# Kernel optimization log

Hardware: AMD Instinct MI355X
Metric: run time of the kernel (lower is better)

Reference implementation:

```python
import jax, jax.numpy as jnp
import numpy as np

B, S, D, H = 2, 2048, 1024, 16
DK = D // H
NEG = -1.0e9


def setup_inputs() -> dict:
    key = jax.random.key(0)
    ks = jax.random.split(key, 11)
    inp = {
        "q": jax.random.normal(ks[0], (B, S, D), jnp.float32),
        "k": jax.random.normal(ks[1], (B, S, D), jnp.float32),
        "v": jax.random.normal(ks[2], (B, S, D), jnp.float32),
        "mask": jnp.tril(jnp.ones((S, S), jnp.int32))[None, None],  # causal [1,1,S,S]
    }
    scale = 0.02
    inp["w_q"] = jax.random.normal(ks[3], (D, D), jnp.float32) * scale
    inp["b_q"] = jnp.zeros((D,), jnp.float32)
    inp["w_k"] = jax.random.normal(ks[4], (D, D), jnp.float32) * scale
    inp["b_k"] = jnp.zeros((D,), jnp.float32)
    inp["w_v"] = jax.random.normal(ks[5], (D, D), jnp.float32) * scale
    inp["b_v"] = jnp.zeros((D,), jnp.float32)
    inp["w_o"] = jax.random.normal(ks[6], (D, D), jnp.float32) * scale
    inp["b_o"] = jnp.zeros((D,), jnp.float32)
    return inp


def reference(q, k, v, mask, w_q, b_q, w_k, b_k, w_v, b_v, w_o, b_o):
    # projections: [B,S,D] -> [B,H,S,DK]
    def proj(x, w, b):
        y = jnp.einsum("bsd,de->bse", x, w) + b
        return y.reshape(B, S, H, DK).transpose(0, 2, 1, 3)

    Q = proj(q, w_q, b_q)
    K = proj(k, w_k, b_k)
    V = proj(v, w_v, b_v)
    # explicit scores matrix, faithful to the original naive attention
    scores = jnp.einsum("bhsd,bhtd->bhst", Q, K) / jnp.sqrt(jnp.float32(DK))
    scores = jnp.where(mask == 0, NEG, scores)
    attn = jax.nn.softmax(scores, axis=-1)  # dropout p=0.0 -> identity
    x = jnp.einsum("bhst,bhtd->bhsd", attn, V)
    x = x.transpose(0, 2, 1, 3).reshape(B, S, D)
    return jnp.einsum("bsd,de->bse", x, w_o) + b_o
```

## Files before the change

### kernel.cpp

```cpp
#include <hip/hip_runtime.h>
#include <hip/hip_bf16.h>

typedef __bf16 bf16;
typedef __bf16 bf16x2 __attribute__((ext_vector_type(2)));
typedef __bf16 bf16x8 __attribute__((ext_vector_type(8)));
typedef float f32x4 __attribute__((ext_vector_type(4)));
typedef float f32x16 __attribute__((ext_vector_type(16)));

#define MFMA16(a, b, c) __builtin_amdgcn_mfma_f32_16x16x32_bf16(a, b, c, 0, 0, 0)
#define MFMA32(a, b, c) __builtin_amdgcn_mfma_f32_32x32x16_bf16(a, b, c, 0, 0, 0)

#define QSCALE 0.18033688f

__global__ __launch_bounds__(256) void convert_k(const float* __restrict__ q,
                                                 const float* __restrict__ k,
                                                 const float* __restrict__ v,
                                                 bf16* __restrict__ qb,
                                                 bf16* __restrict__ kb,
                                                 bf16* __restrict__ vb) {
  const float* src = blockIdx.y == 0 ? q : blockIdx.y == 1 ? k : v;
  bf16* dst = blockIdx.y == 0 ? qb : blockIdx.y == 1 ? kb : vb;
  const size_t i = ((size_t)blockIdx.x * 256 + threadIdx.x) * 8;
  float4 a = *(const float4*)(src + i);
  float4 b = *(const float4*)(src + i + 4);
  bf16x8 o;
  o[0] = (bf16)a.x; o[1] = (bf16)a.y; o[2] = (bf16)a.z; o[3] = (bf16)a.w;
  o[4] = (bf16)b.x; o[5] = (bf16)b.y; o[6] = (bf16)b.z; o[7] = (bf16)b.w;
  *(bf16x8*)(dst + i) = o;
}

__global__ __launch_bounds__(256) void transpose_w(const float* __restrict__ w0,
                                                   const float* __restrict__ w1,
                                                   const float* __restrict__ w2,
                                                   const float* __restrict__ w3,
                                                   bf16* __restrict__ dst) {
  __shared__ bf16 T[64][68];
  const float* W = blockIdx.z == 0 ? w0 : blockIdx.z == 1 ? w1
                   : blockIdx.z == 2 ? w2 : w3;
  bf16* Y = dst + (size_t)blockIdx.z * 1024 * 1024;
  const int t = threadIdx.x, r = t >> 2, c4 = t & 3;
  const int k0 = blockIdx.y * 64, n0 = blockIdx.x * 64;

  const float4* src = (const float4*)(W + (size_t)(k0 + r) * 1024 + n0 + c4 * 16);
  float4 f0 = src[0], f1 = src[1], f2 = src[2], f3 = src[3];
  bf16* row = &T[r][c4 * 16];
  row[0] = (bf16)f0.x; row[1] = (bf16)f0.y; row[2] = (bf16)f0.z; row[3] = (bf16)f0.w;
  row[4] = (bf16)f1.x; row[5] = (bf16)f1.y; row[6] = (bf16)f1.z; row[7] = (bf16)f1.w;
  row[8] = (bf16)f2.x; row[9] = (bf16)f2.y; row[10] = (bf16)f2.z; row[11] = (bf16)f2.w;
  row[12] = (bf16)f3.x; row[13] = (bf16)f3.y; row[14] = (bf16)f3.z; row[15] = (bf16)f3.w;
  __syncthreads();

  bf16x8 o0, o1;
#pragma unroll
  for (int j = 0; j < 8; ++j) o0[j] = T[c4 * 16 + j][r];
#pragma unroll
  for (int j = 0; j < 8; ++j) o1[j] = T[c4 * 16 + 8 + j][r];
  bf16* d = Y + (size_t)(n0 + r) * 1024 + k0 + c4 * 16;
  *(bf16x8*)d = o0;
  *(bf16x8*)(d + 8) = o1;
}

template <int QKV, int MT>
__global__ __launch_bounds__(256, 3) void gemm_p(
    const bf16* __restrict__ xq, const bf16* __restrict__ xk,
    const bf16* __restrict__ xv, const bf16* __restrict__ Wt,
    const float* __restrict__ bq, const float* __restrict__ bk,
    const float* __restrict__ bv, bf16* __restrict__ Qp,
    bf16* __restrict__ Kp, bf16* __restrict__ Vtp, float* __restrict__ Yf) {
  constexpr int AROWS = MT * 32;
  __shared__ bf16 Al[AROWS * 72];
  __shared__ bf16 Bl[128 * 72];

  const int z = QKV ? blockIdx.z : 0;
  const bf16* X = QKV ? (z == 0 ? xq : z == 1 ? xk : xv) : xq;
  const bf16* Bt = Wt + (size_t)z * 1048576;
  const float* bias = QKV ? (z == 0 ? bq : z == 1 ? bk : bv) : bq;
  const float escale = (QKV && z == 0) ? QSCALE : 1.0f;

  const int t = threadIdx.x;
  const int wave = t >> 6, lane = t & 63, quad = lane >> 4, l16 = lane & 15;
  const int wm = (wave >> 1) * (MT * 16), wn = (wave & 1) * 64;
  const int bm = blockIdx.y * AROWS, bn = blockIdx.x * 128;

  constexpr int NA = (MT == 4) ? 4 : 2;
  const int arow = (MT == 4) ? (t >> 1) : (t >> 2);
  const int acol = (MT == 4) ? ((t & 1) * 32) : ((t & 3) * 16);
  const int brow = t >> 1, bcol = (t & 1) * 32;
  const bf16* gA = X + (size_t)(bm + arow) * 1024 + acol;
  const bf16* gB = Bt + (size_t)(bn + brow) * 1024 + bcol;

  bf16x8 ra[NA], rb[4];
#pragma unroll
  for (int j = 0; j < NA; ++j) ra[j] = *(const bf16x8*)(gA + j * 8);
#pragma unroll
  for (int j = 0; j < 4; ++j) rb[j] = *(const bf16x8*)(gB + j * 8);

  f32x4 acc[MT][4] = {};

  for (int kb = 0; kb < 1024; kb += 64) {
    __syncthreads();
#pragma unroll
    for (int j = 0; j < NA; ++j)
      *(bf16x8*)(Al + arow * 72 + acol + j * 8) = ra[j];
#pragma unroll
    for (int j = 0; j < 4; ++j)
      *(bf16x8*)(Bl + brow * 72 + bcol + j * 8) = rb[j];
    __syncthreads();

    if (kb + 64 < 1024) {
#pragma unroll
      for (int j = 0; j < NA; ++j)
        ra[j] = *(const bf16x8*)(gA + kb + 64 + j * 8);
#pragma unroll
      for (int j = 0; j < 4; ++j)
        rb[j] = *(const bf16x8*)(gB + kb + 64 + j * 8);
    }

#pragma unroll
    for (int kk = 0; kk < 2; ++kk) {
      bf16x8 af[MT], bfr[4];
#pragma unroll
      for (int mt = 0; mt < MT; ++mt)
        af[mt] =
            *(const bf16x8*)(Al + (wm + mt * 16 + l16) * 72 + kk * 32 + quad * 8);
#pragma unroll
      for (int nt = 0; nt < 4; ++nt)
        bfr[nt] =
            *(const bf16x8*)(Bl + (wn + nt * 16 + l16) * 72 + kk * 32 + quad * 8);
#pragma unroll
      for (int mt = 0; mt < MT; ++mt)
#pragma unroll
        for (int nt = 0; nt < 4; ++nt)
          acc[mt][nt] = MFMA16(af[mt], bfr[nt], acc[mt][nt]);
    }
  }

  if (QKV && z == 2) {
    bf16* Tt = Al;
    const int b = bm >> 11;
    __syncthreads();
#pragma unroll
    for (int half = 0; half < 2; ++half) {
      if ((wave & 1) == half) {
#pragma unroll
        for (int nt = 0; nt < 4; ++nt) {
          const int ln = nt * 16 + l16;
          const float bia = bias[bn + half * 64 + ln];
#pragma unroll
          for (int mt = 0; mt < 4; ++mt)
#pragma unroll
            for (int r = 0; r < 4; ++r) {
              const int m = wm + mt * 16 + quad * 4 + r;
              Tt[ln * 136 + m] = (bf16)(acc[mt][nt][r] + bia);
            }
        }
      }
      __syncthreads();
      {
        const int ln = t >> 2, seg = (t & 3) * 32;
        const int gn = bn + half * 64 + ln;
        const int h = gn >> 6, dk = gn & 63;
        const int s0 = (bm & 2047) + seg;
        bf16* dstp = Vtp + ((size_t)(b * 16 + h) * 64 + dk) * 2048 + s0;
        const bf16* srcp = Tt + ln * 136 + seg;
#pragma unroll
        for (int j = 0; j < 4; ++j)
          *(bf16x8*)(dstp + j * 8) = *(const bf16x8*)(srcp + j * 8);
      }
      __syncthreads();
    }
  } else {
#pragma unroll
    for (int mt = 0; mt < MT; ++mt)
#pragma unroll
      for (int nt = 0; nt < 4; ++nt) {
        const int gn = bn + wn + nt * 16 + l16;
        const float bia = bias[gn];
#pragma unroll
        for (int r = 0; r < 4; ++r) {
          const int gm = bm + wm + mt * 16 + quad * 4 + r;
          const float val = (acc[mt][nt][r] + bia) * escale;
          if (!QKV) {
            Yf[(size_t)gm * 1024 + gn] = val;
          } else {
            const int b = gm >> 11, s = gm & 2047;
            const int h = gn >> 6, dk = gn & 63;
            bf16* Y = (z == 0) ? Qp : Kp;
            Y[((size_t)(b * 16 + h) * 2048 + s) * 64 + dk] = (bf16)val;
          }
        }
      }
  }
}

__global__ __launch_bounds__(256, 2) void attn_k(const bf16* __restrict__ Q,
                                                 const bf16* __restrict__ K,
                                                 const bf16* __restrict__ Vt,
                                                 bf16* __restrict__ X) {
  __shared__ __align__(16) bf16 Kl[2][64 * 64];
  __shared__ __align__(16) bf16 Vl[2][64 * 64];
  __shared__ float rsL[4][32];

  const int t = threadIdx.x;
  const int wave = t >> 6, lane = t & 63;
  const int cl = lane & 31, h = lane >> 5;

  const int n = blockIdx.x;
  const int xcd = n & 7, mm = n >> 3;
  const int bh = xcd + 8 * (mm & 3);
  const int ii = mm >> 2;
  const int qt = (ii < 8) ? ii : 23 - ii;
  const int ntiles = 2 * qt + 2;
  const int q0 = qt * 128 + wave * 32;
  const int b = bh >> 4, hh = bh & 15;

  const bf16* Qb = Q + (size_t)bh * 2048 * 64;
  const bf16* Kb = K + (size_t)bh * 2048 * 64;
  const bf16* Vb = Vt + (size_t)bh * 64 * 2048;

  bf16x8 qf[4];
#pragma unroll
  for (int ks = 0; ks < 4; ++ks)
    qf[ks] = *(const bf16x8*)(Qb + (size_t)(q0 + cl) * 64 + ks * 16 + h * 8);

  const int sr = t >> 2, sc4 = t & 3;
  const int swz = (sr & 7) << 4;
  const int d0 = sr * 128 + ((sc4 * 32) ^ swz);
  const int d1 = sr * 128 + ((sc4 * 32 + 16) ^ swz);
  const bf16* gK = Kb + sr * 64 + sc4 * 16;
  const bf16* gV = Vb + (size_t)sr * 2048 + sc4 * 16;

  const int fswz = (cl & 7) << 4;

  f32x16 o0 = {}, o1 = {};
  float rs = 0.f;

  {
    bf16x8 ka = *(const bf16x8*)gK;
    bf16x8 kb2 = *(const bf16x8*)(gK + 8);
    bf16x8 va = *(const bf16x8*)gV;
    bf16x8 vb2 = *(const bf16x8*)(gV + 8);
    *(bf16x8*)((char*)Kl[0] + d0) = ka;
    *(bf16x8*)((char*)Kl[0] + d1) = kb2;
    *(bf16x8*)((char*)Vl[0] + d0) = va;
    *(bf16x8*)((char*)Vl[0] + d1) = vb2;
  }
  __syncthreads();

  for (int kt = 0; kt < ntiles; ++kt) {
    const int cur = kt & 1;
    const int k0 = kt * 64;
    const bool more = kt + 1 < ntiles;
    bf16x8 ka, kb2, va, vb2;
    if (more) {
      const bf16* nK = gK + (size_t)(kt + 1) * 4096;
      const bf16* nV = gV + (kt + 1) * 64;
      ka = *(const bf16x8*)nK;
      kb2 = *(const bf16x8*)(nK + 8);
      va = *(const bf16x8*)nV;
      vb2 = *(const bf16x8*)(nV + 8);
    }

    f32x16 s0 = {}, s1 = {};
    const char* Kc = (const char*)Kl[cur];
    __builtin_amdgcn_s_setprio(1);
#pragma unroll
    for (int ks = 0; ks < 4; ++ks) {
      const int cb = ks * 32 + h * 16;
      bf16x8 f0 = *(const bf16x8*)(Kc + cl * 128 + (cb ^ fswz));
      bf16x8 f1 = *(const bf16x8*)(Kc + (cl + 32) * 128 + (cb ^ fswz));
      s0 = MFMA32(f0, qf[ks], s0);
      s1 = MFMA32(f1, qf[ks], s1);
    }
    __builtin_amdgcn_s_setprio(0);

    const bool interior = (k0 + 63) <= q0;
    unsigned pk[8][2];
    float ts = 0.f;
    auto smax = [&](const f32x16& s, int mk) {
#pragma unroll
      for (int sl = 0; sl < 4; ++sl)
#pragma unroll
        for (int p = 0; p < 2; ++p) {
          float e0 = exp2f(s[sl * 4 + 2 * p]);
          float e1 = exp2f(s[sl * 4 + 2 * p + 1]);
          if (!interior) {
            const int ky = k0 + mk * 32 + 8 * sl + 4 * h + 2 * p;
            const int qg = q0 + cl;
            if (ky > qg) e0 = 0.f;
            if (ky + 1 > qg) e1 = 0.f;
          }
          ts += e0 + e1;
          union { bf16x2 v; unsigned u; } cv;
          cv.v[0] = (bf16)e0;
          cv.v[1] = (bf16)e1;
          pk[mk * 4 + sl][p] = cv.u;
        }
    };
    smax(s0, 0);
    smax(s1, 1);
    rs += ts;

    bf16x8 pf[4];
#pragma unroll
    for (int ks = 0; ks < 4; ++ks) {
      const unsigned oe0 = pk[2 * ks][0], oe1 = pk[2 * ks][1];
      const unsigned oo0 = pk[2 * ks + 1][0], oo1 = pk[2 * ks + 1][1];
      const unsigned pe0 = (unsigned)__shfl_xor((int)oe0, 32, 64);
      const unsigned pe1 = (unsigned)__shfl_xor((int)oe1, 32, 64);
      const unsigned po0 = (unsigned)__shfl_xor((int)oo0, 32, 64);
      const unsigned po1 = (unsigned)__shfl_xor((int)oo1, 32, 64);
      union { unsigned u[4]; bf16x8 v; } fu;
      fu.u[0] = h ? po0 : oe0;
      fu.u[1] = h ? po1 : oe1;
      fu.u[2] = h ? oo0 : pe0;
      fu.u[3] = h ? oo1 : pe1;
      pf[ks] = fu.v;
    }

    const char* Vc = (const char*)Vl[cur];
    __builtin_amdgcn_s_setprio(1);
#pragma unroll
    for (int ks = 0; ks < 4; ++ks) {
      const int cb = ks * 32 + h * 16;
      bf16x8 v0f = *(const bf16x8*)(Vc + cl * 128 + (cb ^ fswz));
      bf16x8 v1f = *(const bf16x8*)(Vc + (cl + 32) * 128 + (cb ^ fswz));
      o0 = MFMA32(pf[ks], v0f, o0);
      o1 = MFMA32(pf[ks], v1f, o1);
    }
    __builtin_amdgcn_s_setprio(0);

    if (more) {
      char* Kd = (char*)Kl[cur ^ 1];
      char* Vd = (char*)Vl[cur ^ 1];
      *(bf16x8*)(Kd + d0) = ka;
      *(bf16x8*)(Kd + d1) = kb2;
      *(bf16x8*)(Vd + d0) = va;
      *(bf16x8*)(Vd + d1) = vb2;
    }
    __syncthreads();
  }

  const float rtot = rs + __shfl_xor(rs, 32, 64);
  rsL[wave][cl] = 1.0f / rtot;
  __builtin_amdgcn_s_waitcnt(0xC07F);
  bf16* Xb = X + (size_t)b * 2048 * 1024 + hh * 64;
#pragma unroll
  for (int g = 0; g < 16; ++g) {
    const int qr = (g & 3) + 8 * (g >> 2) + 4 * h;
    const float ri = rsL[wave][qr];
    const int qg = q0 + qr;
    Xb[(size_t)qg * 1024 + cl] = (bf16)(o0[g] * ri);
    Xb[(size_t)qg * 1024 + 32 + cl] = (bf16)(o1[g] * ri);
  }
}

extern "C" void kernel_launch(void* const* d_in, const int* in_sizes, int n_in,
                              void* d_out, int out_size, void* d_ws,
                              size_t ws_size, hipStream_t stream) {
  const float* q = (const float*)d_in[0];
  const float* k = (const float*)d_in[1];
  const float* v = (const float*)d_in[2];
  const float* w_q = (const float*)d_in[4];
  const float* b_q = (const float*)d_in[5];
  const float* w_k = (const float*)d_in[6];
  const float* b_k = (const float*)d_in[7];
  const float* w_v = (const float*)d_in[8];
  const float* b_v = (const float*)d_in[9];
  const float* w_o = (const float*)d_in[10];
  const float* b_o = (const float*)d_in[11];

  bf16* ws = (bf16*)d_ws;
  const size_t NELEM = (size_t)4096 * 1024;
  bf16* Qp = ws;
  bf16* Kp = ws + NELEM;
  bf16* Vtp = ws + 2 * NELEM;
  bf16* Xp = ws + 3 * NELEM;
  bf16* Wt = ws + 4 * NELEM;
  bf16* Wto = Wt + 3145728;
  bf16* qb = Xp;
  bf16* kb = (bf16*)d_out;
  bf16* vb = kb + NELEM;

  convert_k<<<dim3(2048, 3), 256, 0, stream>>>(q, k, v, qb, kb, vb);
  transpose_w<<<dim3(16, 16, 4), 256, 0, stream>>>(w_q, w_k, w_v, w_o, Wt);

  gemm_p<1, 4><<<dim3(8, 32, 3), 256, 0, stream>>>(
      qb, kb, vb, Wt, b_q, b_k, b_v, Qp, Kp, Vtp, nullptr);
  attn_k<<<dim3(512), 256, 0, stream>>>(Qp, Kp, Vtp, Xp);
  gemm_p<0, 2><<<dim3(8, 64), 256, 0, stream>>>(
      Xp, nullptr, nullptr, Wto, b_o, nullptr, nullptr, nullptr, nullptr,
      nullptr, (float*)d_out);
}
```

Baseline: 248.7 us.

## Split attention KV range across wave pairs with paired causal query tiles

Restructures the attention kernel so each block handles 64-row query tiles in two phases, pairing tile i with tile 31-i to balance causal work. Waves are split into two query sub-tiles times two KV halves: each wave pair processes alternating KV tiles, and partial outputs and row sums are merged through shared memory. The aim is more parallelism per query row and better load balance. The cost is extra LDS use (about 72KB), extra barriers and reduction traffic, and the removal of the setprio hints.

```diff
diff --git a/kernel.cpp b/kernel.cpp
--- a/kernel.cpp
+++ b/kernel.cpp
@@ -197,161 +197,202 @@
                                                  const bf16* __restrict__ K,
                                                  const bf16* __restrict__ Vt,
                                                  bf16* __restrict__ X) {
-  __shared__ __align__(16) bf16 Kl[2][64 * 64];
-  __shared__ __align__(16) bf16 Vl[2][64 * 64];
+  __shared__ __align__(16) char LB[65536];
+  __shared__ float Ex[2048];
+  __shared__ float ExR[128];
   __shared__ float rsL[4][32];
+
+  bf16* KB = (bf16*)LB;
+  bf16* VB = (bf16*)(LB + 32768);
 
   const int t = threadIdx.x;
   const int wave = t >> 6, lane = t & 63;
   const int cl = lane & 31, h = lane >> 5;
+  const int qsub = wave & 1, kpart = wave >> 1;
 
   const int n = blockIdx.x;
   const int xcd = n & 7, mm = n >> 3;
   const int bh = xcd + 8 * (mm & 3);
-  const int ii = mm >> 2;
-  const int qt = (ii < 8) ? ii : 23 - ii;
-  const int ntiles = 2 * qt + 2;
-  const int q0 = qt * 128 + wave * 32;
+  const int pairx = mm >> 2;
   const int b = bh >> 4, hh = bh & 15;
 
   const bf16* Qb = Q + (size_t)bh * 2048 * 64;
   const bf16* Kb = K + (size_t)bh * 2048 * 64;
   const bf16* Vb = Vt + (size_t)bh * 64 * 2048;
-
-  bf16x8 qf[4];
-#pragma unroll
-  for (int ks = 0; ks < 4; ++ks)
-    qf[ks] = *(const bf16x8*)(Qb + (size_t)(q0 + cl) * 64 + ks * 16 + h * 8);
 
   const int sr = t >> 2, sc4 = t & 3;
   const int swz = (sr & 7) << 4;
   const int d0 = sr * 128 + ((sc4 * 32) ^ swz);
   const int d1 = sr * 128 + ((sc4 * 32 + 16) ^ swz);
-  const bf16* gK = Kb + sr * 64 + sc4 * 16;
-  const bf16* gV = Vb + (size_t)sr * 2048 + sc4 * 16;
-
   const int fswz = (cl & 7) << 4;
 
-  f32x16 o0 = {}, o1 = {};
-  float rs = 0.f;
-
-  {
-    bf16x8 ka = *(const bf16x8*)gK;
-    bf16x8 kb2 = *(const bf16x8*)(gK + 8);
-    bf16x8 va = *(const bf16x8*)gV;
-    bf16x8 vb2 = *(const bf16x8*)(gV + 8);
-    *(bf16x8*)((char*)Kl[0] + d0) = ka;
-    *(bf16x8*)((char*)Kl[0] + d1) = kb2;
-    *(bf16x8*)((char*)Vl[0] + d0) = va;
-    *(bf16x8*)((char*)Vl[0] + d1) = vb2;
-  }
-  __syncthreads();
-
-  for (int kt = 0; kt < ntiles; ++kt) {
-    const int cur = kt & 1;
-    const int k0 = kt * 64;
-    const bool more = kt + 1 < ntiles;
-    bf16x8 ka, kb2, va, vb2;
-    if (more) {
-      const bf16* nK = gK + (size_t)(kt + 1) * 4096;
-      const bf16* nV = gV + (kt + 1) * 64;
-      ka = *(const bf16x8*)nK;
-      kb2 = *(const bf16x8*)(nK + 8);
-      va = *(const bf16x8*)nV;
-      vb2 = *(const bf16x8*)(nV + 8);
-    }
-
-    f32x16 s0 = {}, s1 = {};
-    const char* Kc = (const char*)Kl[cur];
-    __builtin_amdgcn_s_setprio(1);
-#pragma unroll
-    for (int ks = 0; ks < 4; ++ks) {
-      const int cb = ks * 32 + h * 16;
-      bf16x8 f0 = *(const bf16x8*)(Kc + cl * 128 + (cb ^ fswz));
-      bf16x8 f1 = *(const bf16x8*)(Kc + (cl + 32) * 128 + (cb ^ fswz));
-      s0 = MFMA32(f0, qf[ks], s0);
-      s1 = MFMA32(f1, qf[ks], s1);
-    }
-    __builtin_amdgcn_s_setprio(0);
-
-    const bool interior = (k0 + 63) <= q0;
-    unsigned pk[8][2];
-    float ts = 0.f;
-    auto smax = [&](const f32x16& s, int mk) {
-#pragma unroll
-      for (int sl = 0; sl < 4; ++sl)
+  for (int ph = 0; ph < 2; ++ph) {
+    const int qt = ph ? 31 - pairx : pairx;
+    const int ntiles = qt + 1;
+    const int S = (ntiles + 1) >> 1;
+    const int q0 = qt * 64 + qsub * 32;
+
+    bf16x8 qf[4];
+#pragma unroll
+    for (int ks = 0; ks < 4; ++ks)
+      qf[ks] = *(const bf16x8*)(Qb + (size_t)(q0 + cl) * 64 + ks * 16 + h * 8);
+
+    f32x16 o0 = {}, o1 = {};
+    float rs = 0.f;
+
+#pragma unroll
+    for (int p = 0; p < 2; ++p) {
+      const bf16* gk = Kb + (size_t)(p * 64 + sr) * 64 + sc4 * 16;
+      const bf16* gv = Vb + (size_t)sr * 2048 + p * 64 + sc4 * 16;
+      bf16x8 ka = *(const bf16x8*)gk, kb2 = *(const bf16x8*)(gk + 8);
+      bf16x8 va = *(const bf16x8*)gv, vb2 = *(const bf16x8*)(gv + 8);
+      char* Kd = (char*)(KB + p * 4096);
+      char* Vd = (char*)(VB + p * 4096);
+      *(bf16x8*)(Kd + d0) = ka;  *(bf16x8*)(Kd + d1) = kb2;
+      *(bf16x8*)(Vd + d0) = va;  *(bf16x8*)(Vd + d1) = vb2;
+    }
+    __syncthreads();
+
+    for (int ss = 0; ss < S; ++ss) {
+      const int par = ss & 1;
+      const bool more = (ss + 1) < S;
+      bf16x8 rk[2][2], rv[2][2];
+      if (more) {
 #pragma unroll
         for (int p = 0; p < 2; ++p) {
-          float e0 = exp2f(s[sl * 4 + 2 * p]);
-          float e1 = exp2f(s[sl * 4 + 2 * p + 1]);
-          if (!interior) {
-            const int ky = k0 + mk * 32 + 8 * sl + 4 * h + 2 * p;
-            const int qg = q0 + cl;
-            if (ky > qg) e0 = 0.f;
-            if (ky + 1 > qg) e1 = 0.f;
-          }
-          ts += e0 + e1;
-          union { bf16x2 v; unsigned u; } cv;
-          cv.v[0] = (bf16)e0;
-          cv.v[1] = (bf16)e1;
-          pk[mk * 4 + sl][p] = cv.u;
-        }
-    };
-    smax(s0, 0);
-    smax(s1, 1);
-    rs += ts;
-
-    bf16x8 pf[4];
-#pragma unroll
-    for (int ks = 0; ks < 4; ++ks) {
-      const unsigned oe0 = pk[2 * ks][0], oe1 = pk[2 * ks][1];
-      const unsigned oo0 = pk[2 * ks + 1][0], oo1 = pk[2 * ks + 1][1];
-      const unsigned pe0 = (unsigned)__shfl_xor((int)oe0, 32, 64);
-      const unsigned pe1 = (unsigned)__shfl_xor((int)oe1, 32, 64);
-      const unsigned po0 = (unsigned)__shfl_xor((int)oo0, 32, 64);
-      const unsigned po1 = (unsigned)__shfl_xor((int)oo1, 32, 64);
-      union { unsigned u[4]; bf16x8 v; } fu;
-      fu.u[0] = h ? po0 : oe0;
-      fu.u[1] = h ? po1 : oe1;
-      fu.u[2] = h ? oo0 : pe0;
-      fu.u[3] = h ? oo1 : pe1;
-      pf[ks] = fu.v;
-    }
-
-    const char* Vc = (const char*)Vl[cur];
-    __builtin_amdgcn_s_setprio(1);
-#pragma unroll
-    for (int ks = 0; ks < 4; ++ks) {
-      const int cb = ks * 32 + h * 16;
-      bf16x8 v0f = *(const bf16x8*)(Vc + cl * 128 + (cb ^ fswz));
-      bf16x8 v1f = *(const bf16x8*)(Vc + (cl + 32) * 128 + (cb ^ fswz));
-      o0 = MFMA32(pf[ks], v0f, o0);
-      o1 = MFMA32(pf[ks], v1f, o1);
-    }
-    __builtin_amdgcn_s_setprio(0);
-
-    if (more) {
-      char* Kd = (char*)Kl[cur ^ 1];
-      char* Vd = (char*)Vl[cur ^ 1];
-      *(bf16x8*)(Kd + d0) = ka;
-      *(bf16x8*)(Kd + d1) = kb2;
-      *(bf16x8*)(Vd + d0) = va;
-      *(bf16x8*)(Vd + d1) = vb2;
-    }
-    __syncthreads();
-  }
-
-  const float rtot = rs + __shfl_xor(rs, 32, 64);
-  rsL[wave][cl] = 1.0f / rtot;
-  __builtin_amdgcn_s_waitcnt(0xC07F);
-  bf16* Xb = X + (size_t)b * 2048 * 1024 + hh * 64;
-#pragma unroll
-  for (int g = 0; g < 16; ++g) {
-    const int qr = (g & 3) + 8 * (g >> 2) + 4 * h;
-    const float ri = rsL[wave][qr];
-    const int qg = q0 + qr;
-    Xb[(size_t)qg * 1024 + cl] = (bf16)(o0[g] * ri);
-    Xb[(size_t)qg * 1024 + 32 + cl] = (bf16)(o1[g] * ri);
+          const int kt2 = 2 * (ss + 1) + p;
+          const bf16* gk = Kb + (size_t)kt2 * 4096 + sr * 64 + sc4 * 16;
+          const bf16* gv = Vb + (size_t)sr * 2048 + kt2 * 64 + sc4 * 16;
+          rk[p][0] = *(const bf16x8*)gk;
+          rk[p][1] = *(const bf16x8*)(gk + 8);
+          rv[p][0] = *(const bf16x8*)gv;
+          rv[p][1] = *(const bf16x8*)(gv + 8);
+        }
+      }
+
+      const int kt = 2 * ss + kpart;
+      if (kt < ntiles) {
+        const int k0 = kt * 64;
+        const char* Kc = (const char*)(KB + (par * 2 + kpart) * 4096);
+        const char* Vc = (const char*)(VB + (par * 2 + kpart) * 4096);
+        const bool interior = (k0 + 63) <= q0;
+
+        f32x16 s0v = {}, s1v = {};
+#pragma unroll
+        for (int ks = 0; ks < 4; ++ks) {
+          const int cb = ks * 32 + h * 16;
+          bf16x8 f0 = *(const bf16x8*)(Kc + cl * 128 + (cb ^ fswz));
+          bf16x8 f1 = *(const bf16x8*)(Kc + (cl + 32) * 128 + (cb ^ fswz));
+          s0v = MFMA32(f0, qf[ks], s0v);
+          s1v = MFMA32(f1, qf[ks], s1v);
+        }
+
+        unsigned pk[8][2];
+        float ts = 0.f;
+        auto smax = [&](const f32x16& sv, int mk) {
+#pragma unroll
+          for (int sl = 0; sl < 4; ++sl)
+#pragma unroll
+            for (int p = 0; p < 2; ++p) {
+              float e0 = exp2f(sv[sl * 4 + 2 * p]);
+              float e1 = exp2f(sv[sl * 4 + 2 * p + 1]);
+              if (!interior) {
+                const int ky = k0 + mk * 32 + 8 * sl + 4 * h + 2 * p;
+                const int qg = q0 + cl;
+                if (ky > qg) e0 = 0.f;
+                if (ky + 1 > qg) e1 = 0.f;
+              }
+              ts += e0 + e1;
+              union { bf16x2 v; unsigned u; } cv;
+              cv.v[0] = (bf16)e0;
+              cv.v[1] = (bf16)e1;
+              pk[mk * 4 + sl][p] = cv.u;
+            }
+        };
+        smax(s0v, 0);
+        smax(s1v, 1);
+        rs += ts;
+
+        bf16x8 pf[4];
+#pragma unroll
+        for (int ks = 0; ks < 4; ++ks) {
+          const unsigned oe0 = pk[2 * ks][0], oe1 = pk[2 * ks][1];
+          const unsigned oo0 = pk[2 * ks + 1][0], oo1 = pk[2 * ks + 1][1];
+          const unsigned pe0 = (unsigned)__shfl_xor((int)oe0, 32, 64);
+          const unsigned pe1 = (unsigned)__shfl_xor((int)oe1, 32, 64);
+          const unsigned po0 = (unsigned)__shfl_xor((int)oo0, 32, 64);
+          const unsigned po1 = (unsigned)__shfl_xor((int)oo1, 32, 64);
+          union { unsigned u[4]; bf16x8 v; } fu;
+          fu.u[0] = h ? po0 : oe0;
+          fu.u[1] = h ? po1 : oe1;
+          fu.u[2] = h ? oo0 : pe0;
+          fu.u[3] = h ? oo1 : pe1;
+          pf[ks] = fu.v;
+        }
+
+#pragma unroll
+        for (int ks = 0; ks < 4; ++ks) {
+          const int cb = ks * 32 + h * 16;
+          bf16x8 v0f = *(const bf16x8*)(Vc + cl * 128 + (cb ^ fswz));
+          bf16x8 v1f = *(const bf16x8*)(Vc + (cl + 32) * 128 + (cb ^ fswz));
+          o0 = MFMA32(pf[ks], v0f, o0);
+          o1 = MFMA32(pf[ks], v1f, o1);
+        }
+      }
+
+      if (more) {
+#pragma unroll
+        for (int p = 0; p < 2; ++p) {
+          char* Kd = (char*)(KB + ((par ^ 1) * 2 + p) * 4096);
+          char* Vd = (char*)(VB + ((par ^ 1) * 2 + p) * 4096);
+          *(bf16x8*)(Kd + d0) = rk[p][0];
+          *(bf16x8*)(Kd + d1) = rk[p][1];
+          *(bf16x8*)(Vd + d0) = rv[p][0];
+          *(bf16x8*)(Vd + d1) = rv[p][1];
+        }
+      }
+      __syncthreads();
+    }
+
+    if (kpart == 0) {
+      float* e = Ex + qsub * 1024;
+#pragma unroll
+      for (int i = 0; i < 16; ++i) e[i * 64 + lane] = o0[i];
+      ExR[qsub * 64 + lane] = rs;
+    }
+    __syncthreads();
+    if (kpart == 1) {
+      const float* e = Ex + qsub * 1024;
+#pragma unroll
+      for (int i = 0; i < 16; ++i) o0[i] += e[i * 64 + lane];
+      rs += ExR[qsub * 64 + lane];
+    }
+    __syncthreads();
+    if (kpart == 0) {
+      float* e = Ex + qsub * 1024;
+#pragma unroll
+      for (int i = 0; i < 16; ++i) e[i * 64 + lane] = o1[i];
+    }
+    __syncthreads();
+    if (kpart == 1) {
+      const float* e = Ex + qsub * 1024;
+#pragma unroll
+      for (int i = 0; i < 16; ++i) o1[i] += e[i * 64 + lane];
+
+      const float rtot = rs + __shfl_xor(rs, 32, 64);
+      rsL[wave][cl] = 1.0f / rtot;
+      __builtin_amdgcn_s_waitcnt(0xC07F);
+      bf16* Xb = X + (size_t)b * 2048 * 1024 + hh * 64;
+#pragma unroll
+      for (int g = 0; g < 16; ++g) {
+        const int qr = (g & 3) + 8 * (g >> 2) + 4 * h;
+        const float ri = rsL[wave][qr];
+        const int qg = q0 + qr;
+        Xb[(size_t)qg * 1024 + cl] = (bf16)(o0[g] * ri);
+        Xb[(size_t)qg * 1024 + 32 + cl] = (bf16)(o1[g] * ri);
+      }
+    }
+    __syncthreads();
   }
 }
 
```

Result: faster. 231.7 us (-6.9%).
